# Performance work log

Hardware: AMD Instinct MI355X
Metric: run time of the kernel (lower is better)

The kernel has to match this reference:

```python
import jax, jax.numpy as jnp
import numpy as np

BITS = 11          # codebook bits -> K = 2048 levels
K = 2 ** BITS
EPS = 1e-10
NUM_POINTS = 262144  # B*T flattened code frames
N_CODEBOOKS = 8
NUM_TUPLES = 10
SUBSAMPLE = 2


def setup_inputs() -> dict:
    key = jax.random.key(0)
    inputs = jax.random.randint(key, (NUM_POINTS, N_CODEBOOKS), 0, K, dtype=jnp.int32)
    # emulate np.random.choice(N, subsample, replace=False) per tuple, deterministically
    rng = np.random.default_rng(0)
    dims = np.stack([rng.choice(N_CODEBOOKS, SUBSAMPLE, replace=False) for _ in range(NUM_TUPLES)])
    tuple_dims = jnp.asarray(dims, dtype=jnp.int32)
    return {"inputs": inputs, "tuple_dims": tuple_dims}


def reference(inputs, tuple_dims):
    # inputs: [P, N] int levels; tuple_dims: [T, S] selected codebook indices per tuple
    sub = inputs[:, tuple_dims]              # [P, T, S]
    sub = jnp.transpose(sub, (1, 2, 0))      # [T, S, P]
    T, S, P = sub.shape

    # marginal histograms: [T, S, K] via scatter-add
    def hist1d(v):
        return jnp.zeros((K,), jnp.float32).at[v].add(1.0)
    marg = jax.vmap(jax.vmap(hist1d))(sub)   # [T, S, K]

    # joint index fold: idx = (((v0)*K + v1)*K + ...)
    j = sub[:, 0]                             # [T, P]
    for s in range(1, S):
        j = sub[:, s] + K * j

    def histJ(v):
        return jnp.zeros((K ** S,), jnp.float32).at[v].add(1.0)
    joint = jax.vmap(histJ)(j)                # [T, K^S]

    marg_pdf = marg / jnp.sum(marg, axis=-1, keepdims=True)
    joint_pdf = joint / jnp.sum(joint, axis=-1, keepdims=True)

    H_marg = jnp.sum(-jnp.sum(marg_pdf * jnp.log2(marg_pdf + EPS), axis=-1), axis=-1)  # [T]
    H_joint = -jnp.sum(joint_pdf * jnp.log2(joint_pdf + EPS), axis=-1)                 # [T]
    mi = (H_marg - H_joint) / H_marg          # normalize=True

    return (jnp.mean(mi), jnp.mean(H_marg), jnp.mean(H_joint))
```

## Files before the change

kernel.cpp:

```cpp
#include <hip/hip_runtime.h>
#include <cstdint>
#include <cstddef>

#define KBINS 2048
#define NDIMS 8
#define EPSF 1e-10f
#define MAXT 10
#define BPT 64
#define MARG_BLOCKS 128
#define MARG_WORDS (NDIMS * KBINS / 2)
#define SCAT_BLOCKS 512
#define CAP_CELL 32
#define MENT_BLOCKS (NDIMS * 8)
#define NBMAX (MAXT * BPT)
#define CELL_U32 (NBMAX * CAP_CELL / 2)

__device__ inline float block_reduce_sum(float v) {
#pragma unroll
  for (int off = 32; off > 0; off >>= 1) v += __shfl_down(v, off, 64);
  __shared__ float smem[4];
  int lane = threadIdx.x & 63, wid = threadIdx.x >> 6;
  if (lane == 0) smem[wid] = v;
  __syncthreads();
  if (threadIdx.x == 0) {
    v = smem[0];
    for (int w = 1; w < 4; ++w) v += smem[w];
  }
  return v;
}

__device__ inline int sel8(const int4& a, const int4& b, int d) {
  switch (d) {
    case 0: return a.x;
    case 1: return a.y;
    case 2: return a.z;
    case 3: return a.w;
    case 4: return b.x;
    case 5: return b.y;
    case 6: return b.z;
    default: return b.w;
  }
}

__global__ __launch_bounds__(256) void scatter_marg_hist(
    const int4* __restrict__ in4, const int* __restrict__ tdims,
    uint16_t* __restrict__ bdata, uint32_t* __restrict__ privMarg,
    uint32_t* __restrict__ done, int P, int T) {
  __shared__ uint32_t sh[CELL_U32 + NBMAX];
  __shared__ int sdim[2 * MAXT];
  const int NB = T * BPT;

  if (blockIdx.x == 0 && threadIdx.x == 0) atomicExch(done, 0u);

  if (blockIdx.x < MARG_BLOCKS) {
    uint4* h4 = (uint4*)sh;
    uint4 z; z.x = 0u; z.y = 0u; z.z = 0u; z.w = 0u;
    for (int i = threadIdx.x; i < MARG_WORDS / 4; i += 256) h4[i] = z;
    __syncthreads();
    int per = (P + MARG_BLOCKS - 1) / MARG_BLOCKS;
    int s = blockIdx.x * per, e = min(P, s + per);
    for (int p = s + threadIdx.x; p < e; p += 256) {
      int4 a = in4[2 * p];
      int4 b = in4[2 * p + 1];
      atomicAdd(&sh[0 * 1024 + (a.x >> 1)], 1u << ((a.x & 1) * 16));
      atomicAdd(&sh[1 * 1024 + (a.y >> 1)], 1u << ((a.y & 1) * 16));
      atomicAdd(&sh[2 * 1024 + (a.z >> 1)], 1u << ((a.z & 1) * 16));
      atomicAdd(&sh[3 * 1024 + (a.w >> 1)], 1u << ((a.w & 1) * 16));
      atomicAdd(&sh[4 * 1024 + (b.x >> 1)], 1u << ((b.x & 1) * 16));
      atomicAdd(&sh[5 * 1024 + (b.y >> 1)], 1u << ((b.y & 1) * 16));
      atomicAdd(&sh[6 * 1024 + (b.z >> 1)], 1u << ((b.z & 1) * 16));
      atomicAdd(&sh[7 * 1024 + (b.w >> 1)], 1u << ((b.w & 1) * 16));
    }
    __syncthreads();
    uint4* dst4 = (uint4*)(privMarg + (size_t)blockIdx.x * MARG_WORDS);
    for (int i = threadIdx.x; i < MARG_WORDS / 4; i += 256) dst4[i] = h4[i];
  } else {
    uint16_t* cellS = (uint16_t*)sh;
    uint32_t* cur = sh + CELL_U32;
    for (int i = threadIdx.x; i < NB; i += 256) cur[i] = 1u;
    if (threadIdx.x < 2 * T) sdim[threadIdx.x] = tdims[threadIdx.x];
    __syncthreads();
    int blk = blockIdx.x - MARG_BLOCKS;
    int pA = blk * 512 + threadIdx.x;
#pragma unroll
    for (int j = 0; j < 2; ++j) {
      int p = pA + j * 256;
      if (p < P) {
        int4 a = in4[2 * p];
        int4 b = in4[2 * p + 1];
#pragma unroll
        for (int t = 0; t < MAXT; ++t) {
          if (t < T) {
            uint32_t i0 = (uint32_t)sel8(a, b, sdim[2 * t]);
            uint32_t i1 = (uint32_t)sel8(a, b, sdim[2 * t + 1]);
            uint32_t key22 = i0 * 2048u + i1;
            uint32_t bkt = (uint32_t)t * BPT + (key22 >> 16);
            uint32_t slot = atomicAdd(&cur[bkt], 1u);
            if (slot < CAP_CELL)
              cellS[bkt * CAP_CELL + slot] = (uint16_t)(key22 & 0xffffu);
          }
        }
      }
    }
    __syncthreads();
    for (int c = threadIdx.x; c < NB; c += 256)
      cellS[c * CAP_CELL] = (uint16_t)(cur[c] - 1u);
    __syncthreads();
    uint4* bd4 = (uint4*)bdata;
    const uint4* cs4 = (const uint4*)cellS;
    for (int i = threadIdx.x; i < NB * 4; i += 256) {
      int c = i >> 2, q = i & 3;
      int n = (int)cur[c] - 1;
      if (8 * q <= n)
        bd4[((size_t)c * SCAT_BLOCKS + blk) * 4 + q] = cs4[i];
    }
  }
}

__global__ __launch_bounds__(256) void entropy_fin(
    const uint16_t* __restrict__ bdata, const uint32_t* __restrict__ privMarg,
    float* __restrict__ Hpart, float* __restrict__ HdPart,
    const int* __restrict__ tdims, uint32_t* __restrict__ done, int T,
    float invP, int totalBlocks, float* __restrict__ out) {
  __shared__ uint32_t hist[8192];
  __shared__ uint32_t isLast;
  const int NB = T * BPT;
  float acc = 0.0f;

  if ((int)blockIdx.x < NB) {
    int b = blockIdx.x;
    uint4* h4 = (uint4*)hist;
    uint4 z; z.x = 0u; z.y = 0u; z.z = 0u; z.w = 0u;
    for (int i = threadIdx.x; i < 2048; i += 256) h4[i] = z;
    __syncthreads();
    int blk0 = threadIdx.x, blk1 = threadIdx.x + 256;
    const uint4* c0v = (const uint4*)(bdata + ((size_t)b * SCAT_BLOCKS + blk0) * CAP_CELL);
    const uint4* c1v = (const uint4*)(bdata + ((size_t)b * SCAT_BLOCKS + blk1) * CAP_CELL);
    uint32_t w0[CAP_CELL / 2], w1[CAP_CELL / 2];
    uint4 q0 = c0v[0];
    uint4 q1 = c1v[0];
    w0[0] = q0.x; w0[1] = q0.y; w0[2] = q0.z; w0[3] = q0.w;
    w1[0] = q1.x; w1[1] = q1.y; w1[2] = q1.z; w1[3] = q1.w;
    int n0 = (int)(w0[0] & 0xffffu);
    int n1 = (int)(w1[0] & 0xffffu);
    if (n0 > CAP_CELL - 1) n0 = CAP_CELL - 1;
    if (n1 > CAP_CELL - 1) n1 = CAP_CELL - 1;
    if (n0 >= 8)  { q0 = c0v[1]; w0[4] = q0.x; w0[5] = q0.y; w0[6] = q0.z; w0[7] = q0.w; }
    if (n1 >= 8)  { q1 = c1v[1]; w1[4] = q1.x; w1[5] = q1.y; w1[6] = q1.z; w1[7] = q1.w; }
    if (n0 >= 16) { q0 = c0v[2]; w0[8] = q0.x; w0[9] = q0.y; w0[10] = q0.z; w0[11] = q0.w; }
    if (n1 >= 16) { q1 = c1v[2]; w1[8] = q1.x; w1[9] = q1.y; w1[10] = q1.z; w1[11] = q1.w; }
    if (n0 >= 24) { q0 = c0v[3]; w0[12] = q0.x; w0[13] = q0.y; w0[14] = q0.z; w0[15] = q0.w; }
    if (n1 >= 24) { q1 = c1v[3]; w1[12] = q1.x; w1[13] = q1.y; w1[14] = q1.z; w1[15] = q1.w; }
#pragma unroll
    for (int s = 1; s < CAP_CELL; ++s) {
      if (s <= n0) {
        uint32_t w = w0[s >> 1];
        uint32_t v = (s & 1) ? (w >> 16) : (w & 0xffffu);
        atomicAdd(&hist[v >> 3], 1u << ((v & 7u) * 4u));
      }
    }
#pragma unroll
    for (int s = 1; s < CAP_CELL; ++s) {
      if (s <= n1) {
        uint32_t w = w1[s >> 1];
        uint32_t v = (s & 1) ? (w >> 16) : (w & 0xffffu);
        atomicAdd(&hist[v >> 3], 1u << ((v & 7u) * 4u));
      }
    }
    __syncthreads();
    uint32_t ns1 = 0, ns2 = 0;
#pragma unroll
    for (int s = 1; s < CAP_CELL; ++s) {
      if (s <= n0) {
        uint32_t w = w0[s >> 1];
        uint32_t v = (s & 1) ? (w >> 16) : (w & 0xffffu);
        uint32_t c = (hist[v >> 3] >> ((v & 7u) * 4u)) & 15u;
        if (c == 1u) ++ns1;
        else if (c == 2u) ++ns2;
        else acc += __log2f((float)c * invP + EPSF);
      }
    }
#pragma unroll
    for (int s = 1; s < CAP_CELL; ++s) {
      if (s <= n1) {
        uint32_t w = w1[s >> 1];
        uint32_t v = (s & 1) ? (w >> 16) : (w & 0xffffu);
        uint32_t c = (hist[v >> 3] >> ((v & 7u) * 4u)) & 15u;
        if (c == 1u) ++ns1;
        else if (c == 2u) ++ns2;
        else acc += __log2f((float)c * invP + EPSF);
      }
    }
    acc += (float)ns1 * __log2f(1.0f * invP + EPSF) +
           (float)ns2 * __log2f(2.0f * invP + EPSF);
    acc = block_reduce_sum(acc);
    if (threadIdx.x == 0) atomicExch(&Hpart[blockIdx.x], acc);
  } else {
    int m = blockIdx.x - NB;
    int dim = m >> 3, chunk = m & 7;
    int col = chunk * 128 + (threadIdx.x & 127);
    int half = threadIdx.x >> 7;
    uint32_t lo = 0, hi = 0;
    const uint32_t* base =
        privMarg + (size_t)(half * (MARG_BLOCKS / 2)) * MARG_WORDS + dim * 1024 + col;
#pragma unroll 4
    for (int r = 0; r < MARG_BLOCKS / 2; ++r) {
      uint32_t w = base[(size_t)r * MARG_WORDS];
      lo += w & 0xffffu;
      hi += w >> 16;
    }
    if (half == 1) {
      hist[threadIdx.x & 127] = lo;
      hist[128 + (threadIdx.x & 127)] = hi;
    }
    __syncthreads();
    float la = 0.0f;
    if (half == 0) {
      lo += hist[threadIdx.x];
      hi += hist[128 + threadIdx.x];
      if (lo) { float pz = (float)lo * invP; la += pz * __log2f(pz + EPSF); }
      if (hi) { float pz = (float)hi * invP; la += pz * __log2f(pz + EPSF); }
    }
    la = block_reduce_sum(la);
    if (threadIdx.x == 0) atomicExch(&HdPart[m], la);
  }

  if (threadIdx.x == 0) {
    __threadfence();
    uint32_t old = atomicAdd(done, 1u);
    isLast = (old == (uint32_t)(totalBlocks - 1)) ? 1u : 0u;
  }
  __syncthreads();

  if (isLast) {
    __threadfence();
    float* fh = (float*)hist;
    if (threadIdx.x < MAXT + NDIMS) fh[threadIdx.x] = 0.0f;
    __syncthreads();
    for (int i = threadIdx.x; i < NB; i += 256) {
      float v = atomicAdd(&Hpart[i], 0.0f);
      atomicAdd(&fh[i / BPT], v);
    }
    if (threadIdx.x < MENT_BLOCKS) {
      float v = atomicAdd(&HdPart[threadIdx.x], 0.0f);
      atomicAdd(&fh[MAXT + (threadIdx.x >> 3)], v);
    }
    __syncthreads();
    if (threadIdx.x == 0) {
      float smi = 0.0f, shm = 0.0f, shj = 0.0f;
      for (int t = 0; t < T; ++t) {
        float Hm = -(fh[MAXT + tdims[2 * t]] + fh[MAXT + tdims[2 * t + 1]]);
        float Hjv = -fh[t] * invP;
        smi += (Hm - Hjv) / Hm;
        shm += Hm;
        shj += Hjv;
      }
      float invT = 1.0f / (float)T;
      out[0] = smi * invT;
      out[1] = shm * invT;
      out[2] = shj * invT;
    }
  }
}

extern "C" void kernel_launch(void* const* d_in, const int* in_sizes, int n_in,
                              void* d_out, int out_size, void* d_ws, size_t ws_size,
                              hipStream_t stream) {
  const int* inputs = (const int*)d_in[0];
  const int* tdims = (const int*)d_in[1];
  int P = in_sizes[0] / NDIMS;
  int T = in_sizes[1] / 2;
  if (T > MAXT) T = MAXT;
  float invP = 1.0f / (float)P;
  int NB = T * BPT;

  char* ws = (char*)d_ws;
  uint32_t* done = (uint32_t*)ws;
  size_t off = 4;
  float* HdPart = (float*)(ws + off); off += MENT_BLOCKS * 4;
  float* Hpart = (float*)(ws + off); off += (size_t)MAXT * BPT * 4;
  off = (off + 255) & ~(size_t)255;
  uint32_t* privMarg = (uint32_t*)(ws + off);
  off += (size_t)MARG_BLOCKS * MARG_WORDS * 4;
  off = (off + 255) & ~(size_t)255;
  uint16_t* bdata = (uint16_t*)(ws + off);

  scatter_marg_hist<<<MARG_BLOCKS + SCAT_BLOCKS, 256, 0, stream>>>(
      (const int4*)inputs, tdims, bdata, privMarg, done, P, T);
  entropy_fin<<<NB + MENT_BLOCKS, 256, 0, stream>>>(
      bdata, privMarg, Hpart, HdPart, tdims, done, T, invP,
      NB + MENT_BLOCKS, (float*)d_out);
}
```

Measured before the change: 97.58 us.

## Halve scatter blocks with larger per-cell capacity and one cell per thread

The bucket-scatter stage now uses 256 blocks of 1024 points each instead of 512 blocks of 512, with each per-block bucket cell holding up to 48 keys instead of 32. The finalize stage then reads one cell per thread instead of two. A specialized fully unrolled path is added for the common case T==MAXT. This cuts the number of scatter blocks and the partial-cell writes, and simplifies the finalize loop. The cost is more shared-memory pressure per scatter block, and a higher chance of cell overflow if the bucket distribution is skewed.

```diff
diff --git a/kernel.cpp b/kernel.cpp
--- a/kernel.cpp
+++ b/kernel.cpp
@@ -9,8 +9,9 @@
 #define BPT 64
 #define MARG_BLOCKS 128
 #define MARG_WORDS (NDIMS * KBINS / 2)
-#define SCAT_BLOCKS 512
-#define CAP_CELL 32
+#define SCAT_BLOCKS 256
+#define CAP_CELL 48
+#define CELL_QUADS (CAP_CELL / 8)
 #define MENT_BLOCKS (NDIMS * 8)
 #define NBMAX (MAXT * BPT)
 #define CELL_U32 (NBMAX * CAP_CELL / 2)
@@ -81,16 +82,26 @@
     if (threadIdx.x < 2 * T) sdim[threadIdx.x] = tdims[threadIdx.x];
     __syncthreads();
     int blk = blockIdx.x - MARG_BLOCKS;
-    int pA = blk * 512 + threadIdx.x;
-#pragma unroll
-    for (int j = 0; j < 2; ++j) {
+    int pA = blk * 1024 + threadIdx.x;
+#pragma unroll
+    for (int j = 0; j < 4; ++j) {
       int p = pA + j * 256;
       if (p < P) {
         int4 a = in4[2 * p];
         int4 b = in4[2 * p + 1];
-#pragma unroll
-        for (int t = 0; t < MAXT; ++t) {
-          if (t < T) {
+        if (T == MAXT) {
+#pragma unroll
+          for (int t = 0; t < MAXT; ++t) {
+            uint32_t i0 = (uint32_t)sel8(a, b, sdim[2 * t]);
+            uint32_t i1 = (uint32_t)sel8(a, b, sdim[2 * t + 1]);
+            uint32_t key22 = i0 * 2048u + i1;
+            uint32_t bkt = (uint32_t)t * BPT + (key22 >> 16);
+            uint32_t slot = atomicAdd(&cur[bkt], 1u);
+            if (slot < CAP_CELL)
+              cellS[bkt * CAP_CELL + slot] = (uint16_t)(key22 & 0xffffu);
+          }
+        } else {
+          for (int t = 0; t < T; ++t) {
             uint32_t i0 = (uint32_t)sel8(a, b, sdim[2 * t]);
             uint32_t i1 = (uint32_t)sel8(a, b, sdim[2 * t + 1]);
             uint32_t key22 = i0 * 2048u + i1;
@@ -108,11 +119,11 @@
     __syncthreads();
     uint4* bd4 = (uint4*)bdata;
     const uint4* cs4 = (const uint4*)cellS;
-    for (int i = threadIdx.x; i < NB * 4; i += 256) {
-      int c = i >> 2, q = i & 3;
+    for (int i = threadIdx.x; i < NB * CELL_QUADS; i += 256) {
+      int c = i / CELL_QUADS, q = i - c * CELL_QUADS;
       int n = (int)cur[c] - 1;
       if (8 * q <= n)
-        bd4[((size_t)c * SCAT_BLOCKS + blk) * 4 + q] = cs4[i];
+        bd4[((size_t)c * SCAT_BLOCKS + blk) * CELL_QUADS + q] = cs4[i];
     }
   }
 }
@@ -133,58 +144,33 @@
     uint4 z; z.x = 0u; z.y = 0u; z.z = 0u; z.w = 0u;
     for (int i = threadIdx.x; i < 2048; i += 256) h4[i] = z;
     __syncthreads();
-    int blk0 = threadIdx.x, blk1 = threadIdx.x + 256;
-    const uint4* c0v = (const uint4*)(bdata + ((size_t)b * SCAT_BLOCKS + blk0) * CAP_CELL);
-    const uint4* c1v = (const uint4*)(bdata + ((size_t)b * SCAT_BLOCKS + blk1) * CAP_CELL);
-    uint32_t w0[CAP_CELL / 2], w1[CAP_CELL / 2];
-    uint4 q0 = c0v[0];
-    uint4 q1 = c1v[0];
-    w0[0] = q0.x; w0[1] = q0.y; w0[2] = q0.z; w0[3] = q0.w;
-    w1[0] = q1.x; w1[1] = q1.y; w1[2] = q1.z; w1[3] = q1.w;
-    int n0 = (int)(w0[0] & 0xffffu);
-    int n1 = (int)(w1[0] & 0xffffu);
-    if (n0 > CAP_CELL - 1) n0 = CAP_CELL - 1;
-    if (n1 > CAP_CELL - 1) n1 = CAP_CELL - 1;
-    if (n0 >= 8)  { q0 = c0v[1]; w0[4] = q0.x; w0[5] = q0.y; w0[6] = q0.z; w0[7] = q0.w; }
-    if (n1 >= 8)  { q1 = c1v[1]; w1[4] = q1.x; w1[5] = q1.y; w1[6] = q1.z; w1[7] = q1.w; }
-    if (n0 >= 16) { q0 = c0v[2]; w0[8] = q0.x; w0[9] = q0.y; w0[10] = q0.z; w0[11] = q0.w; }
-    if (n1 >= 16) { q1 = c1v[2]; w1[8] = q1.x; w1[9] = q1.y; w1[10] = q1.z; w1[11] = q1.w; }
-    if (n0 >= 24) { q0 = c0v[3]; w0[12] = q0.x; w0[13] = q0.y; w0[14] = q0.z; w0[15] = q0.w; }
-    if (n1 >= 24) { q1 = c1v[3]; w1[12] = q1.x; w1[13] = q1.y; w1[14] = q1.z; w1[15] = q1.w; }
+    const uint4* cv =
+        (const uint4*)(bdata + ((size_t)b * SCAT_BLOCKS + threadIdx.x) * CAP_CELL);
+    uint32_t w[CAP_CELL / 2];
+    uint4 q = cv[0];
+    w[0] = q.x; w[1] = q.y; w[2] = q.z; w[3] = q.w;
+    int n = (int)(w[0] & 0xffffu);
+    if (n > CAP_CELL - 1) n = CAP_CELL - 1;
+    if (n >= 8)  { q = cv[1]; w[4] = q.x; w[5] = q.y; w[6] = q.z; w[7] = q.w; }
+    if (n >= 16) { q = cv[2]; w[8] = q.x; w[9] = q.y; w[10] = q.z; w[11] = q.w; }
+    if (n >= 24) { q = cv[3]; w[12] = q.x; w[13] = q.y; w[14] = q.z; w[15] = q.w; }
+    if (n >= 32) { q = cv[4]; w[16] = q.x; w[17] = q.y; w[18] = q.z; w[19] = q.w; }
+    if (n >= 40) { q = cv[5]; w[20] = q.x; w[21] = q.y; w[22] = q.z; w[23] = q.w; }
 #pragma unroll
     for (int s = 1; s < CAP_CELL; ++s) {
-      if (s <= n0) {
-        uint32_t w = w0[s >> 1];
-        uint32_t v = (s & 1) ? (w >> 16) : (w & 0xffffu);
+      if (s <= n) {
+        uint32_t ww = w[s >> 1];
+        uint32_t v = (s & 1) ? (ww >> 16) : (ww & 0xffffu);
         atomicAdd(&hist[v >> 3], 1u << ((v & 7u) * 4u));
       }
     }
+    __syncthreads();
+    uint32_t ns1 = 0, ns2 = 0;
 #pragma unroll
     for (int s = 1; s < CAP_CELL; ++s) {
-      if (s <= n1) {
-        uint32_t w = w1[s >> 1];
-        uint32_t v = (s & 1) ? (w >> 16) : (w & 0xffffu);
-        atomicAdd(&hist[v >> 3], 1u << ((v & 7u) * 4u));
-      }
-    }
-    __syncthreads();
-    uint32_t ns1 = 0, ns2 = 0;
-#pragma unroll
-    for (int s = 1; s < CAP_CELL; ++s) {
-      if (s <= n0) {
-        uint32_t w = w0[s >> 1];
-        uint32_t v = (s & 1) ? (w >> 16) : (w & 0xffffu);
-        uint32_t c = (hist[v >> 3] >> ((v & 7u) * 4u)) & 15u;
-        if (c == 1u) ++ns1;
-        else if (c == 2u) ++ns2;
-        else acc += __log2f((float)c * invP + EPSF);
-      }
-    }
-#pragma unroll
-    for (int s = 1; s < CAP_CELL; ++s) {
-      if (s <= n1) {
-        uint32_t w = w1[s >> 1];
-        uint32_t v = (s & 1) ? (w >> 16) : (w & 0xffffu);
+      if (s <= n) {
+        uint32_t ww = w[s >> 1];
+        uint32_t v = (s & 1) ? (ww >> 16) : (ww & 0xffffu);
         uint32_t c = (hist[v >> 3] >> ((v & 7u) * 4u)) & 15u;
         if (c == 1u) ++ns1;
         else if (c == 2u) ++ns2;
@@ -205,9 +191,9 @@
         privMarg + (size_t)(half * (MARG_BLOCKS / 2)) * MARG_WORDS + dim * 1024 + col;
 #pragma unroll 4
     for (int r = 0; r < MARG_BLOCKS / 2; ++r) {
-      uint32_t w = base[(size_t)r * MARG_WORDS];
-      lo += w & 0xffffu;
-      hi += w >> 16;
+      uint32_t ww = base[(size_t)r * MARG_WORDS];
+      lo += ww & 0xffffu;
+      hi += ww >> 16;
     }
     if (half == 1) {
       hist[threadIdx.x & 127] = lo;
```

After: 99.54 us. 1.02x slower.

## Compute joint entropy from packed histogram scan and halve marginal blocks

Applied to the files above, without the earlier changes.

Replaces the per-element second pass over cell entries (looking up counts and summing logs per element) with a scan over the packed 4-bit histogram words. It assumes every element has count 1, then adds a correction only for bins with count of at least 2, skipping words with no such bins. It also specializes the scatter loop for the full tuple count so it fully unrolls, and halves the number of marginal-histogram blocks. The scan reads all 8192 words per block regardless of how many elements that block holds, and fewer marginal blocks means each one does more work.

```diff
diff --git a/kernel.cpp b/kernel.cpp
--- a/kernel.cpp
+++ b/kernel.cpp
@@ -7,7 +7,7 @@
 #define EPSF 1e-10f
 #define MAXT 10
 #define BPT 64
-#define MARG_BLOCKS 128
+#define MARG_BLOCKS 64
 #define MARG_WORDS (NDIMS * KBINS / 2)
 #define SCAT_BLOCKS 512
 #define CAP_CELL 32
@@ -88,9 +88,19 @@
       if (p < P) {
         int4 a = in4[2 * p];
         int4 b = in4[2 * p + 1];
-#pragma unroll
-        for (int t = 0; t < MAXT; ++t) {
-          if (t < T) {
+        if (T == MAXT) {
+#pragma unroll
+          for (int t = 0; t < MAXT; ++t) {
+            uint32_t i0 = (uint32_t)sel8(a, b, sdim[2 * t]);
+            uint32_t i1 = (uint32_t)sel8(a, b, sdim[2 * t + 1]);
+            uint32_t key22 = i0 * 2048u + i1;
+            uint32_t bkt = (uint32_t)t * BPT + (key22 >> 16);
+            uint32_t slot = atomicAdd(&cur[bkt], 1u);
+            if (slot < CAP_CELL)
+              cellS[bkt * CAP_CELL + slot] = (uint16_t)(key22 & 0xffffu);
+          }
+        } else {
+          for (int t = 0; t < T; ++t) {
             uint32_t i0 = (uint32_t)sel8(a, b, sdim[2 * t]);
             uint32_t i1 = (uint32_t)sel8(a, b, sdim[2 * t + 1]);
             uint32_t key22 = i0 * 2048u + i1;
@@ -168,31 +178,21 @@
       }
     }
     __syncthreads();
-    uint32_t ns1 = 0, ns2 = 0;
-#pragma unroll
-    for (int s = 1; s < CAP_CELL; ++s) {
-      if (s <= n0) {
-        uint32_t w = w0[s >> 1];
-        uint32_t v = (s & 1) ? (w >> 16) : (w & 0xffffu);
-        uint32_t c = (hist[v >> 3] >> ((v & 7u) * 4u)) & 15u;
-        if (c == 1u) ++ns1;
-        else if (c == 2u) ++ns2;
-        else acc += __log2f((float)c * invP + EPSF);
-      }
-    }
-#pragma unroll
-    for (int s = 1; s < CAP_CELL; ++s) {
-      if (s <= n1) {
-        uint32_t w = w1[s >> 1];
-        uint32_t v = (s & 1) ? (w >> 16) : (w & 0xffffu);
-        uint32_t c = (hist[v >> 3] >> ((v & 7u) * 4u)) & 15u;
-        if (c == 1u) ++ns1;
-        else if (c == 2u) ++ns2;
-        else acc += __log2f((float)c * invP + EPSF);
-      }
-    }
-    acc += (float)ns1 * __log2f(1.0f * invP + EPSF) +
-           (float)ns2 * __log2f(2.0f * invP + EPSF);
+    const float L1 = __log2f(invP + EPSF);
+    acc = (float)(n0 + n1) * L1;
+    for (int i = threadIdx.x; i < 8192; i += 256) {
+      uint32_t w = hist[i];
+      if (w & 0xEEEEEEEEu) {
+#pragma unroll
+        for (int k = 0; k < 8; ++k) {
+          uint32_t c = (w >> (4 * k)) & 15u;
+          if (c >= 2u) {
+            float cf = (float)c;
+            acc += cf * (__log2f(cf * invP + EPSF) - L1);
+          }
+        }
+      }
+    }
     acc = block_reduce_sum(acc);
     if (threadIdx.x == 0) atomicExch(&Hpart[blockIdx.x], acc);
   } else {
```

Result: no change. 96.08 us (-1.5%).
